# Optimization experiments

Hardware: AMD Instinct MI355X
Metric: run time of the kernel (lower is better)

The kernel has to match this reference:

```python
import jax, jax.numpy as jnp
import numpy as np
from jax import lax

BATCH = 1048576
NUM_DIGITS = 10


def _build_tables():
    # Exact replication of CarryAdderCell.__init__ table construction.
    next_carry = np.zeros((200, 2), dtype=np.float32)
    digit = np.zeros((200, 10), dtype=np.float32)
    for carry in (0, 1):
        for a in range(10):
            for b in range(10):
                idx = carry * 100 + a * 10 + b
                total = a + b + carry
                next_carry[idx, total // 10] = 1.0
                digit[idx, total % 10] = 1.0
    return jnp.asarray(digit), jnp.asarray(next_carry)


def setup_inputs() -> dict:
    key = jax.random.key(0)
    ka, kb = jax.random.split(key)
    a = jax.random.randint(ka, (BATCH, NUM_DIGITS), 0, 10, dtype=jnp.int32)
    b = jax.random.randint(kb, (BATCH, NUM_DIGITS), 0, 10, dtype=jnp.int32)
    digit_table, carry_table = _build_tables()
    return {"a": a, "b": b, "digit_table": digit_table, "carry_table": carry_table}


def reference(a, b, digit_table, carry_table):
    batch = a.shape[0]

    def step(carry_idx, ab):
        a_t, b_t = ab  # [batch] each
        table_idx = carry_idx * 100 + a_t * 10 + b_t  # [batch]
        digit_logits = digit_table[table_idx]          # [batch, 10]
        h_next = carry_table[table_idx]                # [batch, 2]
        next_carry = jnp.argmax(h_next, axis=-1).astype(jnp.int32)
        return next_carry, digit_logits

    # Process least-significant digit first (pos = num_digits-1 .. 0).
    xs = (a[:, ::-1].T, b[:, ::-1].T)  # each [num_digits, batch]
    carry0 = jnp.zeros((batch,), dtype=jnp.int32)  # initial one-hot carry -> argmax 0
    final_carry, logits_lsd = lax.scan(step, carry0, xs)
    # logits_lsd: [num_digits, batch, 10] in LSD-first order -> reverse, move batch first.
    result_10 = jnp.transpose(logits_lsd[::-1], (1, 0, 2))  # [batch, num_digits, 10]
    leading = jax.nn.one_hot(final_carry, 10, dtype=digit_table.dtype)[:, None, :]
    return jnp.concatenate([leading, result_10], axis=1)  # [batch, num_digits+1, 10]
```

## Files before the change

### kernel.cpp

```cpp
#include <hip/hip_runtime.h>


#define ROWS 128
#define THREADS 256
#define FPR 110
#define LDS_FLOATS (ROWS * FPR)
#define LDS_VEC4 (LDS_FLOATS / 4)

__global__ __launch_bounds__(THREADS) void adder_onehot_kernel(
    const int* __restrict__ a, const int* __restrict__ b,
    float* __restrict__ out, int batch) {
    __shared__ __align__(16) float buf[LDS_FLOATS];

    const int t = threadIdx.x;
    const int row0 = blockIdx.x * ROWS;

    float4* buf4 = (float4*)buf;
    const float4 z = make_float4(0.f, 0.f, 0.f, 0.f);
    for (int i = t; i < LDS_VEC4; i += THREADS) buf4[i] = z;

    int dig[11];
    const bool active = (t < ROWS) && (row0 + t < batch);
    if (active) {
        const int* ap = a + (size_t)(row0 + t) * 10;
        const int* bp = b + (size_t)(row0 + t) * 10;
        int av[10], bv[10];
#pragma unroll
        for (int p = 0; p < 10; ++p) av[p] = ap[p];
#pragma unroll
        for (int p = 0; p < 10; ++p) bv[p] = bp[p];
        int carry = 0;
#pragma unroll
        for (int p = 9; p >= 0; --p) {
            int tot = av[p] + bv[p] + carry;
            int c = tot >= 10;
            dig[1 + p] = c ? tot - 10 : tot;
            carry = c;
        }
        dig[0] = carry;
    }
    __syncthreads();

    if (active) {
        float* rb = buf + t * FPR;
#pragma unroll
        for (int pos = 0; pos < 11; ++pos)
            rb[pos * 10 + dig[pos]] = 1.0f;
    }
    __syncthreads();

    const int rows_here = min(ROWS, batch - row0);
    const int total_f = rows_here * FPR;
    const int nvec = total_f / 4;
    float4* out4 = (float4*)(out + (size_t)row0 * FPR);
    for (int i = t; i < nvec; i += THREADS) out4[i] = buf4[i];

    const int tail0 = nvec * 4;
    if (t < total_f - tail0)
        out[(size_t)row0 * FPR + tail0 + t] = buf[tail0 + t];
}

extern "C" void kernel_launch(void* const* d_in, const int* in_sizes, int n_in,
                              void* d_out, int out_size, void* d_ws, size_t ws_size,
                              hipStream_t stream) {
    const int* a = (const int*)d_in[0];
    const int* b = (const int*)d_in[1];
    float* out = (float*)d_out;
    const int batch = in_sizes[0] / 10;

    const int grid = (batch + ROWS - 1) / ROWS;
    adder_onehot_kernel<<<grid, THREADS, 0, stream>>>(a, b, out, batch);
}
```

Baseline: 112.6 us.

## Pack digits into LDS nibbles and synthesize one-hot output on the fly

Replaces the 56KB LDS staging buffer of dense one-hot floats with a small packed per-row digit array of 4-bit nibbles. The store loop decodes each float4's row, position and slot arithmetically and emits 0/1 values directly, removing the LDS zero-fill and scattered writes. Cutting LDS from 56KB to about 1KB allows much higher occupancy for this write-bound kernel, at the cost of extra integer ALU per output vector.

Measured after the change: 112.7 us. About the same (+0.1%).

```diff
diff --git a/kernel.cpp b/kernel.cpp
--- a/kernel.cpp
+++ b/kernel.cpp
@@ -4,24 +4,16 @@
 #define ROWS 128
 #define THREADS 256
 #define FPR 110
-#define LDS_FLOATS (ROWS * FPR)
-#define LDS_VEC4 (LDS_FLOATS / 4)
 
 __global__ __launch_bounds__(THREADS) void adder_onehot_kernel(
     const int* __restrict__ a, const int* __restrict__ b,
     float* __restrict__ out, int batch) {
-    __shared__ __align__(16) float buf[LDS_FLOATS];
+    __shared__ uint2 packed[ROWS + 1];
 
     const int t = threadIdx.x;
     const int row0 = blockIdx.x * ROWS;
 
-    float4* buf4 = (float4*)buf;
-    const float4 z = make_float4(0.f, 0.f, 0.f, 0.f);
-    for (int i = t; i < LDS_VEC4; i += THREADS) buf4[i] = z;
-
-    int dig[11];
-    const bool active = (t < ROWS) && (row0 + t < batch);
-    if (active) {
+    if (t < ROWS && row0 + t < batch) {
         const int* ap = a + (size_t)(row0 + t) * 10;
         const int* bp = b + (size_t)(row0 + t) * 10;
         int av[10], bv[10];
@@ -29,6 +21,8 @@
         for (int p = 0; p < 10; ++p) av[p] = ap[p];
 #pragma unroll
         for (int p = 0; p < 10; ++p) bv[p] = bp[p];
+
+        int dig[11];
         int carry = 0;
 #pragma unroll
         for (int p = 9; p >= 0; --p) {
@@ -38,26 +32,62 @@
             carry = c;
         }
         dig[0] = carry;
-    }
-    __syncthreads();
 
-    if (active) {
-        float* rb = buf + t * FPR;
+        unsigned w0 = 0, w1 = 0;
 #pragma unroll
-        for (int pos = 0; pos < 11; ++pos)
-            rb[pos * 10 + dig[pos]] = 1.0f;
+        for (int pos = 0; pos < 8; ++pos) w0 |= (unsigned)dig[pos] << (4 * pos);
+#pragma unroll
+        for (int pos = 8; pos < 11; ++pos) w1 |= (unsigned)dig[pos] << (4 * (pos - 8));
+        packed[t] = make_uint2(w0, w1);
     }
     __syncthreads();
 
     const int rows_here = min(ROWS, batch - row0);
     const int total_f = rows_here * FPR;
-    const int nvec = total_f / 4;
+    const int nvec = total_f >> 2;
     float4* out4 = (float4*)(out + (size_t)row0 * FPR);
-    for (int i = t; i < nvec; i += THREADS) out4[i] = buf4[i];
+
+    int e0 = 4 * t;
+    int row = e0 / 110;
+    int rem = e0 - 110 * row;
+
+    for (int i = t; i < nvec; i += THREADS) {
+        uint2 p0 = packed[row];
+        uint2 p1 = packed[row + 1];
+        float4 v;
+        float* vp = &v.x;
+#pragma unroll
+        for (int k = 0; k < 4; ++k) {
+            int re = rem + k;
+            bool wrap = re >= 110;
+            int re2 = wrap ? re - 110 : re;
+            unsigned wlo = wrap ? p1.x : p0.x;
+            unsigned whi = wrap ? p1.y : p0.y;
+            int pos = (re2 * 205) >> 11;
+            int slot = re2 - 10 * pos;
+            unsigned w = (pos >= 8) ? whi : wlo;
+            int digit = (w >> ((pos & 7) * 4)) & 15;
+            vp[k] = (digit == slot) ? 1.0f : 0.0f;
+        }
+        out4[i] = v;
+
+        row += 9;
+        rem += 34;
+        if (rem >= 110) { rem -= 110; ++row; }
+    }
 
     const int tail0 = nvec * 4;
-    if (t < total_f - tail0)
-        out[(size_t)row0 * FPR + tail0 + t] = buf[tail0 + t];
+    if (t < total_f - tail0) {
+        int e = tail0 + t;
+        int r = e / 110;
+        int re2 = e - 110 * r;
+        int pos = (re2 * 205) >> 11;
+        int slot = re2 - 10 * pos;
+        uint2 pw = packed[r];
+        unsigned w = (pos >= 8) ? pw.y : pw.x;
+        int digit = (w >> ((pos & 7) * 4)) & 15;
+        out[(size_t)row0 * FPR + e] = (digit == slot) ? 1.0f : 0.0f;
+    }
 }
 
 extern "C" void kernel_launch(void* const* d_in, const int* in_sizes, int n_in,
```
